# Kernel tuning notes

Measured on AMD Instinct MI355X. Metric: run time of the kernel, lower is better.

## Reference

```python
import jax, jax.numpy as jnp
import numpy as np


def setup_inputs() -> dict:
    key = jax.random.key(0)
    k1, k2 = jax.random.split(key)
    B, L = 4096, 8192
    inputs = jax.random.normal(k1, (B, L), dtype=jnp.float32)
    filters = jax.random.normal(k2, (B, L), dtype=jnp.float32)
    return {"inputs": inputs, "filters": filters}


def reference(inputs, filters):
    L = inputs.shape[-1]
    n = 2 * L  # zero-pad to 2L for linear (non-circular) convolution
    # rfft with norm='forward' scales by 1/n; irfft with norm='forward' scales by n.
    x_f = jnp.fft.rfft(inputs, n=n, axis=-1, norm="forward")
    h_f = jnp.fft.rfft(filters, n=n, axis=-1, norm="forward")
    y = jnp.fft.irfft(x_f * h_f, n=n, axis=-1, norm="forward")
    return y[..., :L]
```

## Files before the change

### kernel.cpp

```cpp
#include <hip/hip_runtime.h>

#define TPB 1024
#define NFFT 16384
#define LROW 8192
#define LDSN 17408

typedef float v2f __attribute__((ext_vector_type(2)));

__device__ __forceinline__ v2f mk(float x, float y) { v2f r; r.x = x; r.y = y; return r; }
__device__ __forceinline__ v2f sp(float x) { return mk(x, x); }
__device__ __forceinline__ v2f ineg(v2f a) { return mk(a.y, -a.x); }
__device__ __forceinline__ v2f ipos(v2f a) { return mk(-a.y, a.x); }

struct twd { v2f cc, ss; };
__device__ __forceinline__ twd mktw(float c, float s) { twd w; w.cc = sp(c); w.ss = sp(s); return w; }
__device__ __forceinline__ v2f ap(v2f a, twd w) { return a * w.cc + ipos(a) * w.ss; }
__device__ __forceinline__ twd twsq(twd w) {
  twd r; r.cc = w.cc * w.cc - w.ss * w.ss; v2f t = w.cc * w.ss; r.ss = t + t; return r;
}
__device__ __forceinline__ twd twmul(twd a, twd b) {
  twd r; r.cc = a.cc * b.cc - a.ss * b.ss; r.ss = a.ss * b.cc + a.cc * b.ss; return r;
}

#define C16 0.923879532511287f
#define S16 0.382683432365090f
#define R2H 0.70710678118655f

__device__ __forceinline__ twd rotf(twd w) {
  twd r; r.cc = w.cc * sp(C16) + w.ss * sp(S16); r.ss = w.ss * sp(C16) - w.cc * sp(S16); return r;
}
__device__ __forceinline__ twd roti(twd w) {
  twd r; r.cc = w.cc * sp(C16) - w.ss * sp(S16); r.ss = w.ss * sp(C16) + w.cc * sp(S16); return r;
}

__device__ __forceinline__ int pad(int p) { return p + (p >> 4); }

__device__ __forceinline__ int rev4_14(int p) {
  unsigned r = __brev((unsigned)p) >> 18;
  return (int)(((r & 0x1555u) << 1) | ((r & 0x2AAAu) >> 1));
}

__device__ __forceinline__ void sc_rev(float rev, float& c, float& s) {
  s = __builtin_amdgcn_sinf(rev);
  c = __builtin_amdgcn_cosf(rev);
}

__device__ __forceinline__ void dif_core(v2f& a0, v2f& a1, v2f& a2, v2f& a3) {
  v2f t0 = a0 + a2, t1 = a0 - a2;
  v2f t2 = a1 + a3, t3 = a1 - a3;
  v2f u = ineg(t3);
  a0 = t0 + t2;
  a1 = t1 + u;
  a2 = t0 - t2;
  a3 = t1 - u;
}

__device__ __forceinline__ void dit_core(v2f& a0, v2f& a1, v2f& a2, v2f& a3) {
  v2f t0 = a0 + a2, t1 = a0 - a2;
  v2f t2 = a1 + a3, t3 = a1 - a3;
  v2f u = ineg(t3);
  a0 = t0 + t2;
  a1 = t1 - u;
  a2 = t0 - t2;
  a3 = t1 + u;
}

__device__ __forceinline__ void fwd_first(const float* __restrict__ xr,
                                          const float* __restrict__ hr,
                                          v2f* __restrict__ z, int t) {
  v2f X[4][4];
  #pragma unroll
  for (int e = 0; e < 4; e++) {
    #pragma unroll
    for (int d = 0; d < 2; d++) {
      int p = t + 1024 * e + 4096 * d;
      X[e][d] = mk(xr[p], hr[p]);
    }
  }
  float c1, s1;
  sc_rev(-(float)t * (1.0f / 16384.0f), c1, s1);
  twd w1 = mktw(c1, s1);
  #pragma unroll
  for (int e = 0; e < 4; e++) {
    if (e) w1 = rotf(w1);
    v2f a0 = X[e][0], a1 = X[e][1];
    v2f u = ineg(a1);
    v2f y1 = a0 + u;
    v2f y2 = a0 - a1;
    v2f y3 = a0 - u;
    twd w2 = twsq(w1), w3 = twmul(w2, w1);
    X[e][0] = a0 + a1;
    X[e][1] = ap(y1, w1);
    X[e][2] = ap(y2, w2);
    X[e][3] = ap(y3, w3);
  }
  float cb, sb;
  sc_rev(-(float)t * (1.0f / 4096.0f), cb, sb);
  twd wb1 = mktw(cb, sb), wb2 = twsq(wb1), wb3 = twmul(wb2, wb1);
  #pragma unroll
  for (int d = 0; d < 4; d++) {
    dif_core(X[0][d], X[1][d], X[2][d], X[3][d]);
    X[1][d] = ap(X[1][d], wb1);
    X[2][d] = ap(X[2][d], wb2);
    X[3][d] = ap(X[3][d], wb3);
  }
  const int lb = t + (t >> 4);
  #pragma unroll
  for (int e = 0; e < 4; e++)
    #pragma unroll
    for (int d = 0; d < 4; d++)
      z[lb + 1088 * e + 4352 * d] = X[e][d];
}

template <int n>
__device__ __forceinline__ void fwd_pair(v2f* __restrict__ z, int t) {
  constexpr int q = n >> 2;
  constexpr int qp = n >> 4;
  constexpr int OE = qp + (qp >> 4);
  constexpr int OD = q + (q >> 4);
  const int jp = t & (qp - 1);
  const int G = (t & ~(qp - 1)) << 4;
  const int lb = G + (G >> 4) + jp + (jp >> 4);
  v2f X[4][4];
  #pragma unroll
  for (int e = 0; e < 4; e++)
    #pragma unroll
    for (int d = 0; d < 4; d++)
      X[e][d] = z[lb + e * OE + d * OD];
  float c1, s1;
  sc_rev(-(float)jp / (float)n, c1, s1);
  twd w1 = mktw(c1, s1);
  #pragma unroll
  for (int e = 0; e < 4; e++) {
    if (e) w1 = rotf(w1);
    dif_core(X[e][0], X[e][1], X[e][2], X[e][3]);
    twd w2 = twsq(w1), w3 = twmul(w2, w1);
    X[e][1] = ap(X[e][1], w1);
    X[e][2] = ap(X[e][2], w2);
    X[e][3] = ap(X[e][3], w3);
  }
  float cb, sb;
  sc_rev(-(float)jp / (float)q, cb, sb);
  twd wb1 = mktw(cb, sb), wb2 = twsq(wb1), wb3 = twmul(wb2, wb1);
  #pragma unroll
  for (int d = 0; d < 4; d++) {
    dif_core(X[0][d], X[1][d], X[2][d], X[3][d]);
    X[1][d] = ap(X[1][d], wb1);
    X[2][d] = ap(X[2][d], wb2);
    X[3][d] = ap(X[3][d], wb3);
  }
  #pragma unroll
  for (int e = 0; e < 4; e++)
    #pragma unroll
    for (int d = 0; d < 4; d++)
      z[lb + e * OE + d * OD] = X[e][d];
}

__device__ __forceinline__ void fwd_last(v2f* __restrict__ z, int t) {
  const int lb = 17 * t;
  #pragma unroll
  for (int u = 0; u < 4; u++) {
    v2f a0 = z[lb + 4 * u + 0];
    v2f a1 = z[lb + 4 * u + 1];
    v2f a2 = z[lb + 4 * u + 2];
    v2f a3 = z[lb + 4 * u + 3];
    dif_core(a0, a1, a2, a3);
    z[lb + 4 * u + 0] = a0;
    z[lb + 4 * u + 1] = a1;
    z[lb + 4 * u + 2] = a2;
    z[lb + 4 * u + 3] = a3;
  }
}

__device__ __forceinline__ void untangle(v2f* __restrict__ z, int t) {
  const float SC = 3.7252902984619141e-09f;
  const float SC4 = 9.3132257461547852e-10f;
  #pragma unroll
  for (int it = 0; it < 8; it++) {
    int b = t + it * TPB;
    if (b == 0) {
      v2f z0 = z[0];
      z[0] = mk(z0.x * z0.y * SC, 0.f);
      v2f zm = z[2];
      z[2] = mk(zm.x * zm.y * SC, 0.f);
    } else {
      int p = ((b >> 1) << 2) | (b & 1);
      int k = rev4_14(p);
      int pn = rev4_14(NFFT - k);
      int a = pad(p), apn = pad(pn);
      v2f zk = z[a];
      v2f zn = z[apn];
      float Pr = zk.x + zn.x, Pi = zk.y - zn.y;
      float Qr = zk.x - zn.x, Qi = zk.y + zn.y;
      float pqr = Pr * Qr - Pi * Qi;
      float pqi = Pr * Qi + Pi * Qr;
      float Sr = pqi * SC4, Si = -pqr * SC4;
      z[a] = mk(Sr, Si);
      z[apn] = mk(Sr, -Si);
    }
  }
}

__device__ __forceinline__ void inv_first(v2f* __restrict__ z, int t) {
  const int lb = 17 * t;
  v2f X[4][4];
  #pragma unroll
  for (int e = 0; e < 4; e++)
    #pragma unroll
    for (int d = 0; d < 4; d++)
      X[e][d] = z[lb + e + 4 * d];
  #pragma unroll
  for (int d = 0; d < 4; d++)
    dit_core(X[0][d], X[1][d], X[2][d], X[3][d]);
  const twd wA = {sp(C16), sp(S16)};
  const twd wB = {sp(R2H), sp(R2H)};
  const twd wC = {sp(S16), sp(C16)};
  const twd wD = {sp(-R2H), sp(R2H)};
  const twd wE = {sp(-C16), sp(-S16)};
  dit_core(X[0][0], X[0][1], X[0][2], X[0][3]);
  X[1][1] = ap(X[1][1], wA);
  X[1][2] = ap(X[1][2], wB);
  X[1][3] = ap(X[1][3], wC);
  dit_core(X[1][0], X[1][1], X[1][2], X[1][3]);
  X[2][1] = ap(X[2][1], wB);
  X[2][2] = ipos(X[2][2]);
  X[2][3] = ap(X[2][3], wD);
  dit_core(X[2][0], X[2][1], X[2][2], X[2][3]);
  X[3][1] = ap(X[3][1], wC);
  X[3][2] = ap(X[3][2], wD);
  X[3][3] = ap(X[3][3], wE);
  dit_core(X[3][0], X[3][1], X[3][2], X[3][3]);
  #pragma unroll
  for (int e = 0; e < 4; e++)
    #pragma unroll
    for (int d = 0; d < 4; d++)
      z[lb + e + 4 * d] = X[e][d];
}

template <int nA>
__device__ __forceinline__ void inv_pair(v2f* __restrict__ z, int t) {
  constexpr int qA = nA >> 2;
  constexpr int nB = nA << 2;
  constexpr int OE = qA + (qA >> 4);
  constexpr int OD = nA + (nA >> 4);
  const int jA = t & (qA - 1);
  const int GB = (t & ~(qA - 1)) << 4;
  const int lb = GB + (GB >> 4) + jA + (jA >> 4);
  v2f X[4][4];
  #pragma unroll
  for (int e = 0; e < 4; e++)
    #pragma unroll
    for (int d = 0; d < 4; d++)
      X[e][d] = z[lb + e * OE + d * OD];
  float c1, s1;
  sc_rev((float)jA / (float)nA, c1, s1);
  twd w1 = mktw(c1, s1), w2 = twsq(w1), w3 = twmul(w2, w1);
  #pragma unroll
  for (int d = 0; d < 4; d++) {
    X[1][d] = ap(X[1][d], w1);
    X[2][d] = ap(X[2][d], w2);
    X[3][d] = ap(X[3][d], w3);
    dit_core(X[0][d], X[1][d], X[2][d], X[3][d]);
  }
  float cb, sb;
  sc_rev((float)jA / (float)nB, cb, sb);
  twd wb = mktw(cb, sb);
  #pragma unroll
  for (int e = 0; e < 4; e++) {
    if (e) wb = roti(wb);
    twd wb2 = twsq(wb), wb3 = twmul(wb2, wb);
    X[e][1] = ap(X[e][1], wb);
    X[e][2] = ap(X[e][2], wb2);
    X[e][3] = ap(X[e][3], wb3);
    dit_core(X[e][0], X[e][1], X[e][2], X[e][3]);
  }
  #pragma unroll
  for (int e = 0; e < 4; e++)
    #pragma unroll
    for (int d = 0; d < 4; d++)
      z[lb + e * OE + d * OD] = X[e][d];
}

__device__ __forceinline__ void inv_last_store(const v2f* __restrict__ z,
                                               float* __restrict__ orow, int t) {
  const int lb = t + (t >> 4);
  #pragma unroll
  for (int u = 0; u < 4; u++) {
    int j = t + 1024 * u;
    v2f a0 = z[lb + 1088 * u + 4352 * 0];
    v2f a1 = z[lb + 1088 * u + 4352 * 1];
    v2f a2 = z[lb + 1088 * u + 4352 * 2];
    v2f a3 = z[lb + 1088 * u + 4352 * 3];
    float c1, s1;
    sc_rev((float)j * (1.0f / 16384.0f), c1, s1);
    float c2 = c1 * c1 - s1 * s1, s2 = 2.f * c1 * s1;
    float c3 = c2 * c1 - s2 * s1, s3 = s2 * c1 + c2 * s1;
    float b1r = a1.x * c1 - a1.y * s1, b1i = a1.x * s1 + a1.y * c1;
    float b2r = a2.x * c2 - a2.y * s2;
    float b3r = a3.x * c3 - a3.y * s3, b3i = a3.x * s3 + a3.y * c3;
    float t0r = a0.x + b2r, t1r = a0.x - b2r;
    float t2r = b1r + b3r, t3i = b1i - b3i;
    orow[j] = t0r + t2r;
    orow[j + 4096] = t1r - t3i;
  }
}

extern "C" __global__ void __launch_bounds__(TPB, 4)
fftconv_kernel(const float* __restrict__ x, const float* __restrict__ h,
               float* __restrict__ out) {
  extern __shared__ v2f z[];
  const int t = threadIdx.x;
  const long long row = blockIdx.x;
  const float* xr = x + row * LROW;
  const float* hr = h + row * LROW;

  fwd_first(xr, hr, z, t);  __syncthreads();
  fwd_pair<1024>(z, t);     __syncthreads();
  fwd_pair<64>(z, t);       __syncthreads();
  fwd_last(z, t);           __syncthreads();
  untangle(z, t);           __syncthreads();
  inv_first(z, t);          __syncthreads();
  inv_pair<64>(z, t);       __syncthreads();
  inv_pair<1024>(z, t);     __syncthreads();
  inv_last_store(z, out + row * LROW, t);
}

extern "C" void kernel_launch(void* const* d_in, const int* in_sizes, int n_in,
                              void* d_out, int out_size, void* d_ws, size_t ws_size,
                              hipStream_t stream) {
  const float* x = (const float*)d_in[0];
  const float* h = (const float*)d_in[1];
  float* out = (float*)d_out;
  const int rows = out_size / LROW;
  const size_t lds_bytes = (size_t)LDSN * sizeof(v2f);
  (void)hipFuncSetAttribute((const void*)fftconv_kernel,
                            hipFuncAttributeMaxDynamicSharedMemorySize,
                            (int)lds_bytes);
  hipLaunchKernelGGL(fftconv_kernel, dim3(rows), dim3(TPB), lds_bytes, stream,
                     x, h, out);
}
```

Measured before the change: 485.2 us.

## Fuse last forward radix, spectral product, and first inverse radix via squaring

The separate untangle step paired bins k and N-k to pull out X·H. It is replaced by a pointwise -i·Z² per bin, relying on the packed signal z = x + i·h: the real part of ifft(-i·Z²) scaled by one half equals x⊛h. This makes the spectral step local to each thread's registers. The last forward radix-4 pass, the product and the first inverse radix-16 pass are then fused into one mid_round. That removes two LDS round trips, two barriers and the scattered bit-reversed pair accesses. It relies on the inverse store keeping only the real part, and the x² − h² cross term may cost some numerical precision.

```diff
diff --git a/kernel.cpp b/kernel.cpp
--- a/kernel.cpp
+++ b/kernel.cpp
@@ -31,13 +31,6 @@
 }
 __device__ __forceinline__ twd roti(twd w) {
   twd r; r.cc = w.cc * sp(C16) - w.ss * sp(S16); r.ss = w.ss * sp(C16) + w.cc * sp(S16); return r;
-}
-
-__device__ __forceinline__ int pad(int p) { return p + (p >> 4); }
-
-__device__ __forceinline__ int rev4_14(int p) {
-  unsigned r = __brev((unsigned)p) >> 18;
-  return (int)(((r & 0x1555u) << 1) | ((r & 0x2AAAu) >> 1));
 }
 
 __device__ __forceinline__ void sc_rev(float rev, float& c, float& s) {
@@ -156,85 +149,52 @@
       z[lb + e * OE + d * OD] = X[e][d];
 }
 
-__device__ __forceinline__ void fwd_last(v2f* __restrict__ z, int t) {
+__device__ __forceinline__ void mid_round(v2f* __restrict__ z, int t) {
   const int lb = 17 * t;
-  #pragma unroll
-  for (int u = 0; u < 4; u++) {
-    v2f a0 = z[lb + 4 * u + 0];
-    v2f a1 = z[lb + 4 * u + 1];
-    v2f a2 = z[lb + 4 * u + 2];
-    v2f a3 = z[lb + 4 * u + 3];
-    dif_core(a0, a1, a2, a3);
-    z[lb + 4 * u + 0] = a0;
-    z[lb + 4 * u + 1] = a1;
-    z[lb + 4 * u + 2] = a2;
-    z[lb + 4 * u + 3] = a3;
-  }
-}
-
-__device__ __forceinline__ void untangle(v2f* __restrict__ z, int t) {
-  const float SC = 3.7252902984619141e-09f;
-  const float SC4 = 9.3132257461547852e-10f;
-  #pragma unroll
-  for (int it = 0; it < 8; it++) {
-    int b = t + it * TPB;
-    if (b == 0) {
-      v2f z0 = z[0];
-      z[0] = mk(z0.x * z0.y * SC, 0.f);
-      v2f zm = z[2];
-      z[2] = mk(zm.x * zm.y * SC, 0.f);
-    } else {
-      int p = ((b >> 1) << 2) | (b & 1);
-      int k = rev4_14(p);
-      int pn = rev4_14(NFFT - k);
-      int a = pad(p), apn = pad(pn);
-      v2f zk = z[a];
-      v2f zn = z[apn];
-      float Pr = zk.x + zn.x, Pi = zk.y - zn.y;
-      float Qr = zk.x - zn.x, Qi = zk.y + zn.y;
-      float pqr = Pr * Qr - Pi * Qi;
-      float pqi = Pr * Qi + Pi * Qr;
-      float Sr = pqi * SC4, Si = -pqr * SC4;
-      z[a] = mk(Sr, Si);
-      z[apn] = mk(Sr, -Si);
+  v2f R[4][4];
+  #pragma unroll
+  for (int u = 0; u < 4; u++)
+    #pragma unroll
+    for (int v = 0; v < 4; v++)
+      R[v][u] = z[lb + 4 * u + v];
+  #pragma unroll
+  for (int u = 0; u < 4; u++)
+    dif_core(R[0][u], R[1][u], R[2][u], R[3][u]);
+  const float s  = 1.8626451492309570e-09f;
+  const float s2 = 3.7252902984619141e-09f;
+  #pragma unroll
+  for (int v = 0; v < 4; v++)
+    #pragma unroll
+    for (int u = 0; u < 4; u++) {
+      v2f a = R[v][u];
+      R[v][u] = mk(s2 * a.x * a.y, s * (a.y * a.y - a.x * a.x));
     }
-  }
-}
-
-__device__ __forceinline__ void inv_first(v2f* __restrict__ z, int t) {
-  const int lb = 17 * t;
-  v2f X[4][4];
-  #pragma unroll
-  for (int e = 0; e < 4; e++)
-    #pragma unroll
-    for (int d = 0; d < 4; d++)
-      X[e][d] = z[lb + e + 4 * d];
-  #pragma unroll
-  for (int d = 0; d < 4; d++)
-    dit_core(X[0][d], X[1][d], X[2][d], X[3][d]);
+  #pragma unroll
+  for (int u = 0; u < 4; u++)
+    dit_core(R[0][u], R[1][u], R[2][u], R[3][u]);
   const twd wA = {sp(C16), sp(S16)};
   const twd wB = {sp(R2H), sp(R2H)};
   const twd wC = {sp(S16), sp(C16)};
   const twd wD = {sp(-R2H), sp(R2H)};
   const twd wE = {sp(-C16), sp(-S16)};
-  dit_core(X[0][0], X[0][1], X[0][2], X[0][3]);
-  X[1][1] = ap(X[1][1], wA);
-  X[1][2] = ap(X[1][2], wB);
-  X[1][3] = ap(X[1][3], wC);
-  dit_core(X[1][0], X[1][1], X[1][2], X[1][3]);
-  X[2][1] = ap(X[2][1], wB);
-  X[2][2] = ipos(X[2][2]);
-  X[2][3] = ap(X[2][3], wD);
-  dit_core(X[2][0], X[2][1], X[2][2], X[2][3]);
-  X[3][1] = ap(X[3][1], wC);
-  X[3][2] = ap(X[3][2], wD);
-  X[3][3] = ap(X[3][3], wE);
-  dit_core(X[3][0], X[3][1], X[3][2], X[3][3]);
-  #pragma unroll
-  for (int e = 0; e < 4; e++)
-    #pragma unroll
-    for (int d = 0; d < 4; d++)
-      z[lb + e + 4 * d] = X[e][d];
+  dit_core(R[0][0], R[0][1], R[0][2], R[0][3]);
+  R[1][1] = ap(R[1][1], wA);
+  R[1][2] = ap(R[1][2], wB);
+  R[1][3] = ap(R[1][3], wC);
+  dit_core(R[1][0], R[1][1], R[1][2], R[1][3]);
+  R[2][1] = ap(R[2][1], wB);
+  R[2][2] = ipos(R[2][2]);
+  R[2][3] = ap(R[2][3], wD);
+  dit_core(R[2][0], R[2][1], R[2][2], R[2][3]);
+  R[3][1] = ap(R[3][1], wC);
+  R[3][2] = ap(R[3][2], wD);
+  R[3][3] = ap(R[3][3], wE);
+  dit_core(R[3][0], R[3][1], R[3][2], R[3][3]);
+  #pragma unroll
+  for (int u = 0; u < 4; u++)
+    #pragma unroll
+    for (int v = 0; v < 4; v++)
+      z[lb + 4 * u + v] = R[v][u];
 }
 
 template <int nA>
@@ -317,9 +277,7 @@
   fwd_first(xr, hr, z, t);  __syncthreads();
   fwd_pair<1024>(z, t);     __syncthreads();
   fwd_pair<64>(z, t);       __syncthreads();
-  fwd_last(z, t);           __syncthreads();
-  untangle(z, t);           __syncthreads();
-  inv_first(z, t);          __syncthreads();
+  mid_round(z, t);          __syncthreads();
   inv_pair<64>(z, t);       __syncthreads();
   inv_pair<1024>(z, t);     __syncthreads();
   inv_last_store(z, out + row * LROW, t);
```

After: 453.5 us. -6.5%, faster.
